# Kernel tuning notes

Measured on AMD Instinct MI355X. Metric: run time of the kernel, lower is better.

## Reference

```python
import jax, jax.numpy as jnp
import numpy as np

TEMPERATURE = 8.0  # sqrt(d_k), d_k = 64
MINIMUM_VALUE = -1e9  # stand-in for C.MINIMUM_VALUE


def setup_inputs() -> dict:
    key = jax.random.key(0)
    kq, kk, kv, km = jax.random.split(key, 4)
    B, N, D = 32, 2048, 64
    q = jax.random.normal(kq, (B, N, D), dtype=jnp.float32)
    k = jax.random.normal(kk, (B, N, D), dtype=jnp.float32)
    v = jax.random.normal(kv, (B, N, D), dtype=jnp.float32)
    mask = jax.random.randint(km, (B, N, N), 0, 2, dtype=jnp.int32)
    return {"q": q, "k": k, "v": v, "mask": mask}


def reference(q, k, v, mask):
    # scores: [B, Nq, Nk]
    attn = jnp.einsum("bqd,bkd->bqk", q, k) / TEMPERATURE
    attn = jnp.where(mask > 0, attn, MINIMUM_VALUE)
    attn = jax.nn.softmax(attn, axis=-1)
    # dropout is identity in eval / deterministic reference
    output = jnp.einsum("bqk,bkd->bqd", attn, v)
    return (output, attn)
```

## Files before the change

### kernel.cpp

```cpp
#include <hip/hip_runtime.h>

#define NB 32
#define NN 2048
#define ND 64
#define ROWS 16
#define NBLK (NB * NN / ROWS)

#define LDS_PART 65536
#define LDS_AUX  66048
#define LDS_TOTAL 70144

typedef _Float16 half8 __attribute__((ext_vector_type(8)));
typedef float f32x4 __attribute__((ext_vector_type(4)));

union H4 { uint2 u; _Float16 h[4]; };

__device__ __forceinline__ f32x4 mfma16(half8 a, half8 b, f32x4 c) {
    return __builtin_amdgcn_mfma_f32_16x16x32_f16(a, b, c, 0, 0, 0);
}

__global__ __launch_bounds__(256) void cvt_f32_f16_k(const float* __restrict__ src,
                                                     _Float16* __restrict__ dst) {
    int i = blockIdx.x * 256 + threadIdx.x;
    const f32x4* s = (const f32x4*)src;
    f32x4 a = s[2 * i], b = s[2 * i + 1];
    half8 h;
    h[0] = (_Float16)a[0]; h[1] = (_Float16)a[1]; h[2] = (_Float16)a[2]; h[3] = (_Float16)a[3];
    h[4] = (_Float16)b[0]; h[5] = (_Float16)b[1]; h[6] = (_Float16)b[2]; h[7] = (_Float16)b[3];
    ((half8*)dst)[i] = h;
}

__global__ __launch_bounds__(256) void transpose_v_k(const float* __restrict__ v,
                                                     _Float16* __restrict__ vt) {
    __shared__ float tile[64][65];
    int b = blockIdx.x >> 5;
    int k0 = (blockIdx.x & 31) * 64;
    int t = threadIdx.x;
    {
        int dc = t & 15, kr = t >> 4;
        const f32x4* vp = (const f32x4*)(v + ((size_t)(b * NN + k0) * ND));
        #pragma unroll
        for (int i = 0; i < 4; ++i) {
            int kk = kr + i * 16;
            f32x4 x = vp[kk * 16 + dc];
            tile[kk][dc * 4 + 0] = x[0]; tile[kk][dc * 4 + 1] = x[1];
            tile[kk][dc * 4 + 2] = x[2]; tile[kk][dc * 4 + 3] = x[3];
        }
    }
    __syncthreads();
    {
        int d = t >> 2, ks = (t & 3) * 16;
        union { _Float16 hh[16]; uint4 u4[2]; } pk;
        #pragma unroll
        for (int j = 0; j < 16; ++j) pk.hh[j] = (_Float16)tile[ks + j][d];
        uint4* op = (uint4*)(vt + ((size_t)(b * ND + d) * NN + k0 + ks));
        op[0] = pk.u4[0]; op[1] = pk.u4[1];
    }
}

__global__ __launch_bounds__(512, 4) void attn_main_k(
        const _Float16* __restrict__ qh, const _Float16* __restrict__ kh,
        const _Float16* __restrict__ vtp, const int* __restrict__ mask,
        float* __restrict__ outp, float* __restrict__ attnp) {
    extern __shared__ char smem[];

    int bid = blockIdx.x;
    int lin = (bid & 7) * (NBLK / 8) + (bid >> 3);
    int b  = lin >> 7;
    int q0 = (lin & 127) * ROWS;

    int t = threadIdx.x;
    int w = t >> 6, l = t & 63;
    int l15 = l & 15, lg = l >> 4;
    int sw = (l15 & 7) << 4;

    const _Float16* qb = qh + ((size_t)(b * NN + q0 + l15) * ND) + lg * 8;
    half8 qf0 = *(const half8*)(qb);
    half8 qf1 = *(const half8*)(qb + 32);

    const _Float16* kp = kh + (size_t)b * NN * ND + (size_t)l15 * ND + lg * 8;
    const int* mp = mask + ((size_t)(b * NN + q0 + l15)) * NN + lg * 4;
    char* srow = smem + l15 * 4096;

    int4 mq[4];
    half8 kq0[2], kq1[2];
    #pragma unroll
    for (int d = 0; d < 4; ++d) mq[d] = *(const int4*)(mp + w * 16 + d * 128);
    #pragma unroll
    for (int d = 0; d < 2; ++d) {
        const _Float16* kk = kp + (size_t)(w * 16 + d * 128) * ND;
        kq0[d] = *(const half8*)(kk);
        kq1[d] = *(const half8*)(kk + 32);
    }
    float rsum = 0.f;
    #pragma unroll
    for (int i = 0; i < 16; ++i) {
        int key0 = w * 16 + i * 128;
        int4 mk = mq[i & 3];
        half8 ka = kq0[i & 1], kb = kq1[i & 1];
        if (i + 4 < 16) mq[i & 3] = *(const int4*)(mp + key0 + 512);
        if (i + 2 < 16) {
            const _Float16* kk = kp + (size_t)(key0 + 256) * ND;
            kq0[i & 1] = *(const half8*)(kk);
            kq1[i & 1] = *(const half8*)(kk + 32);
        }
        f32x4 acc = {0.f, 0.f, 0.f, 0.f};
        acc = mfma16(ka, qf0, acc);
        acc = mfma16(kb, qf1, acc);
        float e0 = mk.x > 0 ? __expf(acc[0] * 0.125f) : 0.f;
        float e1 = mk.y > 0 ? __expf(acc[1] * 0.125f) : 0.f;
        float e2 = mk.z > 0 ? __expf(acc[2] * 0.125f) : 0.f;
        float e3 = mk.w > 0 ? __expf(acc[3] * 0.125f) : 0.f;
        rsum += (e0 + e1) + (e2 + e3);
        H4 y;
        y.h[0] = (_Float16)e0; y.h[1] = (_Float16)e1;
        y.h[2] = (_Float16)e2; y.h[3] = (_Float16)e3;
        *(uint2*)(srow + (((key0 + lg * 4) * 2) ^ sw)) = y.u;
    }
    rsum += __shfl_xor(rsum, 16);
    rsum += __shfl_xor(rsum, 32);
    float* part = (float*)(smem + LDS_PART);
    if (l < 16) part[w * 16 + l] = rsum;
    __syncthreads();

    {
        int r = t >> 5, g = t & 31;
        float su = 0.f;
        #pragma unroll
        for (int pw = 0; pw < 8; ++pw) su += part[pw * 16 + r];
        float linv = 1.0f / (su + 1e-37f);
        char* s2 = smem + r * 4096;
        int sw2 = (r & 7) << 4;
        float* arow = attnp + ((size_t)(b * NN + q0 + r)) * NN;
        #pragma unroll
        for (int j = 0; j < 16; ++j) {
            int colb = g * 8 + j * 256;
            H4 x; x.u = *(const uint2*)(s2 + (colb ^ sw2));
            f32x4 av;
            av[0] = (float)x.h[0] * linv;
            av[1] = (float)x.h[1] * linv;
            av[2] = (float)x.h[2] * linv;
            av[3] = (float)x.h[3] * linv;
            *(f32x4*)(arow + (colb >> 1)) = av;
        }
    }

    {
        int ct = w & 3, kseg = w >> 2;
        const _Float16* vp = vtp + (size_t)(b * ND + ct * 16 + l15) * NN + lg * 8;
        char* pbase = smem + l15 * 4096;
        f32x4 o = {0.f, 0.f, 0.f, 0.f};
        #pragma unroll 4
        for (int kk = 0; kk < 32; ++kk) {
            int ks = kseg * 32 + kk;
            half8 pa = *(const half8*)(pbase + ((ks * 64 + lg * 16) ^ sw));
            half8 vb = *(const half8*)(vp + (size_t)ks * 32);
            o = mfma16(pa, vb, o);
        }
        if (kseg) *(f32x4*)(smem + LDS_AUX + ((size_t)((w - 4) * 64 + l)) * 16) = o;
        __syncthreads();
        if (!kseg) {
            f32x4 o2 = *(const f32x4*)(smem + LDS_AUX + ((size_t)(w * 64 + l)) * 16);
            o += o2;
            float* ob = outp + ((size_t)(b * NN + q0 + lg * 4)) * ND + ct * 16 + l15;
            #pragma unroll
            for (int rr = 0; rr < 4; ++rr) {
                int qr = lg * 4 + rr;
                float s8 = 0.f;
                #pragma unroll
                for (int pw = 0; pw < 8; ++pw) s8 += part[pw * 16 + qr];
                ob[(size_t)rr * ND] = o[rr] / (s8 + 1e-37f);
            }
        }
    }
}

extern "C" void kernel_launch(void* const* d_in, const int* in_sizes, int n_in,
                              void* d_out, int out_size, void* d_ws, size_t ws_size,
                              hipStream_t stream) {
    const float* q = (const float*)d_in[0];
    const float* k = (const float*)d_in[1];
    const float* v = (const float*)d_in[2];
    const int* mask = (const int*)d_in[3];
    float* outp  = (float*)d_out;
    float* attnp = outp + (size_t)NB * NN * ND;

    _Float16* qh = (_Float16*)d_ws;
    _Float16* kh = qh + (size_t)NB * NN * ND;
    _Float16* vth = kh + (size_t)NB * NN * ND;

    cvt_f32_f16_k<<<2048, 256, 0, stream>>>(q, qh);
    cvt_f32_f16_k<<<2048, 256, 0, stream>>>(k, kh);
    transpose_v_k<<<1024, 256, 0, stream>>>(v, vth);
    attn_main_k<<<NBLK, 512, LDS_TOTAL, stream>>>(qh, kh, vth, mask, outp, attnp);
}
```

Measured before the change: 444.7 us.

## Pack mask to bits in prepass, hand-schedule K/V loads, nontemporal stores

Adds a pre-kernel that packs the int32 mask into per-lane 64-bit bitmasks, so the main attention kernel reads 8 bytes per lane instead of streaming int32 mask values. The QK and PV loops become macro-unrolled double-buffered register batches separated by sched_barriers to force load/compute overlap. Attention and output stores become nontemporal. The extra kernel still reads the full 512MB mask, so total mask traffic is unchanged; the gain relies on better overlap and cheaper writes, at the cost of an extra launch and workspace.

```diff
diff --git a/kernel.cpp b/kernel.cpp
--- a/kernel.cpp
+++ b/kernel.cpp
@@ -12,12 +12,14 @@
 
 typedef _Float16 half8 __attribute__((ext_vector_type(8)));
 typedef float f32x4 __attribute__((ext_vector_type(4)));
+typedef int i32x4 __attribute__((ext_vector_type(4)));
 
 union H4 { uint2 u; _Float16 h[4]; };
 
 __device__ __forceinline__ f32x4 mfma16(half8 a, half8 b, f32x4 c) {
     return __builtin_amdgcn_mfma_f32_16x16x32_f16(a, b, c, 0, 0, 0);
 }
+#define SB() __builtin_amdgcn_sched_barrier(0)
 
 __global__ __launch_bounds__(256) void cvt_f32_f16_k(const float* __restrict__ src,
                                                      _Float16* __restrict__ dst) {
@@ -58,9 +60,79 @@
     }
 }
 
+__global__ __launch_bounds__(256) void mask_pack_k(const int* __restrict__ mask,
+                                                   unsigned long long* __restrict__ pm) {
+    size_t gid = (size_t)blockIdx.x * 256 + threadIdx.x;
+    size_t row = gid >> 5;
+    int w = ((int)gid >> 2) & 7, lg = (int)gid & 3;
+    const i32x4* mp = (const i32x4*)(mask + row * NN + w * 16 + lg * 4);
+    unsigned long long bits = 0ull;
+    #pragma unroll
+    for (int i = 0; i < 16; i += 4) {
+        i32x4 m0 = __builtin_nontemporal_load(mp + (size_t)(i + 0) * 32);
+        i32x4 m1 = __builtin_nontemporal_load(mp + (size_t)(i + 1) * 32);
+        i32x4 m2 = __builtin_nontemporal_load(mp + (size_t)(i + 2) * 32);
+        i32x4 m3 = __builtin_nontemporal_load(mp + (size_t)(i + 3) * 32);
+        unsigned b0 = (m0[0] > 0 ? 1u : 0u) | (m0[1] > 0 ? 2u : 0u) | (m0[2] > 0 ? 4u : 0u) | (m0[3] > 0 ? 8u : 0u);
+        unsigned b1 = (m1[0] > 0 ? 1u : 0u) | (m1[1] > 0 ? 2u : 0u) | (m1[2] > 0 ? 4u : 0u) | (m1[3] > 0 ? 8u : 0u);
+        unsigned b2 = (m2[0] > 0 ? 1u : 0u) | (m2[1] > 0 ? 2u : 0u) | (m2[2] > 0 ? 4u : 0u) | (m2[3] > 0 ? 8u : 0u);
+        unsigned b3 = (m3[0] > 0 ? 1u : 0u) | (m3[1] > 0 ? 2u : 0u) | (m3[2] > 0 ? 4u : 0u) | (m3[3] > 0 ? 8u : 0u);
+        bits |= (unsigned long long)(b0 | (b1 << 4) | (b2 << 8) | (b3 << 12)) << (i * 4);
+    }
+    pm[gid] = bits;
+}
+
+#define LDK(S, base) { \
+    const _Float16* kk_ = kp + (size_t)(base) * (128 * ND); \
+    S##0a = *(const half8*)(kk_);                S##0b = *(const half8*)(kk_ + 32); \
+    S##1a = *(const half8*)(kk_ + 128 * ND);     S##1b = *(const half8*)(kk_ + 128 * ND + 32); \
+    S##2a = *(const half8*)(kk_ + 2 * 128 * ND); S##2b = *(const half8*)(kk_ + 2 * 128 * ND + 32); \
+    S##3a = *(const half8*)(kk_ + 3 * 128 * ND); S##3b = *(const half8*)(kk_ + 3 * 128 * ND + 32); }
+
+#define CMP1(i, ka_, kb_) { \
+    f32x4 acc = {0.f, 0.f, 0.f, 0.f}; \
+    acc = mfma16(ka_, qf0, acc); \
+    acc = mfma16(kb_, qf1, acc); \
+    unsigned mb = (unsigned)(pmask >> ((i) * 4)) & 15u; \
+    float e0 = (mb & 1u) ? __expf(acc[0] * 0.125f) : 0.f; \
+    float e1 = (mb & 2u) ? __expf(acc[1] * 0.125f) : 0.f; \
+    float e2 = (mb & 4u) ? __expf(acc[2] * 0.125f) : 0.f; \
+    float e3 = (mb & 8u) ? __expf(acc[3] * 0.125f) : 0.f; \
+    rsum += (e0 + e1) + (e2 + e3); \
+    H4 y_; y_.h[0] = (_Float16)e0; y_.h[1] = (_Float16)e1; \
+    y_.h[2] = (_Float16)e2; y_.h[3] = (_Float16)e3; \
+    *(uint2*)(srow + ((((w * 16 + (i) * 128) + lg * 4) * 2) ^ sw)) = y_.u; }
+
+#define CMP4(S, c) { CMP1((c)*4 + 0, S##0a, S##0b) CMP1((c)*4 + 1, S##1a, S##1b) \
+                     CMP1((c)*4 + 2, S##2a, S##2b) CMP1((c)*4 + 3, S##3a, S##3b) }
+
+#define LDV(S, base) { \
+    const _Float16* vv_ = vp + (size_t)(kseg * 32 + (base)) * 32; \
+    S##0 = *(const half8*)(vv_);       S##1 = *(const half8*)(vv_ + 32); \
+    S##2 = *(const half8*)(vv_ + 64);  S##3 = *(const half8*)(vv_ + 96); \
+    S##4 = *(const half8*)(vv_ + 128); S##5 = *(const half8*)(vv_ + 160); \
+    S##6 = *(const half8*)(vv_ + 192); S##7 = *(const half8*)(vv_ + 224); }
+
+#define PV1(ks_, vb_) { \
+    half8 pa_ = *(const half8*)(pbase + ((((ks_) * 64) + lg * 16) ^ sw)); \
+    o = mfma16(pa_, vb_, o); }
+
+#define PV8(S, base) { PV1(kseg*32 + (base) + 0, S##0) PV1(kseg*32 + (base) + 1, S##1) \
+                       PV1(kseg*32 + (base) + 2, S##2) PV1(kseg*32 + (base) + 3, S##3) \
+                       PV1(kseg*32 + (base) + 4, S##4) PV1(kseg*32 + (base) + 5, S##5) \
+                       PV1(kseg*32 + (base) + 6, S##6) PV1(kseg*32 + (base) + 7, S##7) }
+
+#define NRM(jj) { \
+    int colb_ = g * 8 + (jj) * 256; \
+    H4 x_; x_.u = *(const uint2*)(s2 + (colb_ ^ sw2)); \
+    f32x4 av_; \
+    av_[0] = (float)x_.h[0] * linv; av_[1] = (float)x_.h[1] * linv; \
+    av_[2] = (float)x_.h[2] * linv; av_[3] = (float)x_.h[3] * linv; \
+    __builtin_nontemporal_store(av_, (f32x4*)(arow + (colb_ >> 1))); }
+
 __global__ __launch_bounds__(512, 4) void attn_main_k(
         const _Float16* __restrict__ qh, const _Float16* __restrict__ kh,
-        const _Float16* __restrict__ vtp, const int* __restrict__ mask,
+        const _Float16* __restrict__ vtp, const unsigned long long* __restrict__ pm,
         float* __restrict__ outp, float* __restrict__ attnp) {
     extern __shared__ char smem[];
 
@@ -78,45 +150,23 @@
     half8 qf0 = *(const half8*)(qb);
     half8 qf1 = *(const half8*)(qb + 32);
 
-    const _Float16* kp = kh + (size_t)b * NN * ND + (size_t)l15 * ND + lg * 8;
-    const int* mp = mask + ((size_t)(b * NN + q0 + l15)) * NN + lg * 4;
+    unsigned long long pmask = pm[((size_t)(b * NN + q0 + l15) * 8 + w) * 4 + lg];
+
+    const _Float16* kp = kh + (size_t)b * NN * ND + (size_t)(w * 16 + l15) * ND + lg * 8;
     char* srow = smem + l15 * 4096;
 
-    int4 mq[4];
-    half8 kq0[2], kq1[2];
-    #pragma unroll
-    for (int d = 0; d < 4; ++d) mq[d] = *(const int4*)(mp + w * 16 + d * 128);
-    #pragma unroll
-    for (int d = 0; d < 2; ++d) {
-        const _Float16* kk = kp + (size_t)(w * 16 + d * 128) * ND;
-        kq0[d] = *(const half8*)(kk);
-        kq1[d] = *(const half8*)(kk + 32);
-    }
+    half8 A0a, A0b, A1a, A1b, A2a, A2b, A3a, A3b;
+    half8 B0a, B0b, B1a, B1b, B2a, B2b, B3a, B3b;
     float rsum = 0.f;
-    #pragma unroll
-    for (int i = 0; i < 16; ++i) {
-        int key0 = w * 16 + i * 128;
-        int4 mk = mq[i & 3];
-        half8 ka = kq0[i & 1], kb = kq1[i & 1];
-        if (i + 4 < 16) mq[i & 3] = *(const int4*)(mp + key0 + 512);
-        if (i + 2 < 16) {
-            const _Float16* kk = kp + (size_t)(key0 + 256) * ND;
-            kq0[i & 1] = *(const half8*)(kk);
-            kq1[i & 1] = *(const half8*)(kk + 32);
-        }
-        f32x4 acc = {0.f, 0.f, 0.f, 0.f};
-        acc = mfma16(ka, qf0, acc);
-        acc = mfma16(kb, qf1, acc);
-        float e0 = mk.x > 0 ? __expf(acc[0] * 0.125f) : 0.f;
-        float e1 = mk.y > 0 ? __expf(acc[1] * 0.125f) : 0.f;
-        float e2 = mk.z > 0 ? __expf(acc[2] * 0.125f) : 0.f;
-        float e3 = mk.w > 0 ? __expf(acc[3] * 0.125f) : 0.f;
-        rsum += (e0 + e1) + (e2 + e3);
-        H4 y;
-        y.h[0] = (_Float16)e0; y.h[1] = (_Float16)e1;
-        y.h[2] = (_Float16)e2; y.h[3] = (_Float16)e3;
-        *(uint2*)(srow + (((key0 + lg * 4) * 2) ^ sw)) = y.u;
-    }
+    LDK(A, 0)  SB();
+    LDK(B, 4)  SB();
+    CMP4(A, 0) SB();
+    LDK(A, 8)  SB();
+    CMP4(B, 1) SB();
+    LDK(B, 12) SB();
+    CMP4(A, 2) SB();
+    CMP4(B, 3)
+
     rsum += __shfl_xor(rsum, 16);
     rsum += __shfl_xor(rsum, 32);
     float* part = (float*)(smem + LDS_PART);
@@ -132,17 +182,10 @@
         char* s2 = smem + r * 4096;
         int sw2 = (r & 7) << 4;
         float* arow = attnp + ((size_t)(b * NN + q0 + r)) * NN;
-        #pragma unroll
-        for (int j = 0; j < 16; ++j) {
-            int colb = g * 8 + j * 256;
-            H4 x; x.u = *(const uint2*)(s2 + (colb ^ sw2));
-            f32x4 av;
-            av[0] = (float)x.h[0] * linv;
-            av[1] = (float)x.h[1] * linv;
-            av[2] = (float)x.h[2] * linv;
-            av[3] = (float)x.h[3] * linv;
-            *(f32x4*)(arow + (colb >> 1)) = av;
-        }
+        NRM(0)  NRM(1)  NRM(2)  NRM(3)
+        NRM(4)  NRM(5)  NRM(6)  NRM(7)
+        NRM(8)  NRM(9)  NRM(10) NRM(11)
+        NRM(12) NRM(13) NRM(14) NRM(15)
     }
 
     {
@@ -150,13 +193,17 @@
         const _Float16* vp = vtp + (size_t)(b * ND + ct * 16 + l15) * NN + lg * 8;
         char* pbase = smem + l15 * 4096;
         f32x4 o = {0.f, 0.f, 0.f, 0.f};
-        #pragma unroll 4
-        for (int kk = 0; kk < 32; ++kk) {
-            int ks = kseg * 32 + kk;
-            half8 pa = *(const half8*)(pbase + ((ks * 64 + lg * 16) ^ sw));
-            half8 vb = *(const half8*)(vp + (size_t)ks * 32);
-            o = mfma16(pa, vb, o);
-        }
+        half8 V0, V1, V2, V3, V4, V5, V6, V7;
+        half8 W0, W1, W2, W3, W4, W5, W6, W7;
+        LDV(V, 0)   SB();
+        LDV(W, 8)   SB();
+        PV8(V, 0)   SB();
+        LDV(V, 16)  SB();
+        PV8(W, 8)   SB();
+        LDV(W, 24)  SB();
+        PV8(V, 16)  SB();
+        PV8(W, 24)
+
         if (kseg) *(f32x4*)(smem + LDS_AUX + ((size_t)((w - 4) * 64 + l)) * 16) = o;
         __syncthreads();
         if (!kseg) {
@@ -169,7 +216,7 @@
                 float s8 = 0.f;
                 #pragma unroll
                 for (int pw = 0; pw < 8; ++pw) s8 += part[pw * 16 + qr];
-                ob[(size_t)rr * ND] = o[rr] / (s8 + 1e-37f);
+                __builtin_nontemporal_store(o[rr] / (s8 + 1e-37f), ob + (size_t)rr * ND);
             }
         }
     }
@@ -188,9 +235,11 @@
     _Float16* qh = (_Float16*)d_ws;
     _Float16* kh = qh + (size_t)NB * NN * ND;
     _Float16* vth = kh + (size_t)NB * NN * ND;
+    unsigned long long* pm = (unsigned long long*)(vth + (size_t)NB * NN * ND);
 
     cvt_f32_f16_k<<<2048, 256, 0, stream>>>(q, qh);
     cvt_f32_f16_k<<<2048, 256, 0, stream>>>(k, kh);
     transpose_v_k<<<1024, 256, 0, stream>>>(v, vth);
-    attn_main_k<<<NBLK, 512, LDS_TOTAL, stream>>>(qh, kh, vth, mask, outp, attnp);
-}
+    mask_pack_k<<<8192, 256, 0, stream>>>(mask, pm);
+    attn_main_k<<<NBLK, 512, LDS_TOTAL, stream>>>(qh, kh, vth, pm, outp, attnp);
+}
```

Result: faster. 370.0 us (-16.8%).
